# Kernel tuning notes

Measured on AMD Instinct MI355X. Metric: run time of the kernel, lower is better.

## Reference

```python
import jax, jax.numpy as jnp
import numpy as np

B, N, F_IN, F_OUT = 1024, 16, 1024, 4096  # n_nodes=16 and n_heads=1 are structurally fixed by the module


def setup_inputs() -> dict:
    key = jax.random.key(0)
    ks = jax.random.split(key, 7)
    s1 = 1.0 / np.sqrt(F_IN)
    s2 = 1.0 / np.sqrt(F_IN * 16)
    return {
        "x": jax.random.normal(ks[0], (B, N, F_IN), jnp.float32),
        "matrix": jax.random.uniform(ks[1], (B, N, N), jnp.float32),
        "W1": jax.random.uniform(ks[2], (F_IN, F_IN), jnp.float32, -s1, s1),
        "b1": jax.random.uniform(ks[3], (F_IN,), jnp.float32, -s1, s1),
        "W_mlp": jax.random.uniform(ks[4], (F_OUT, F_IN * 16), jnp.float32, -s2, s2),
        "b_mlp": jax.random.uniform(ks[5], (F_OUT,), jnp.float32, -s2, s2),
        "a_param": jnp.float32(5.0),
    }


def _l2norm(v):
    # matches F.normalize(p=2, dim=-1, eps=1e-12)
    n = jnp.maximum(jnp.linalg.norm(v, axis=-1, keepdims=True), 1e-12)
    return v / n


def _forward(x, matrix, W1, b1, W_mlp, b_mlp, a_param):
    Bc, n, f = x.shape  # n_heads = 1, n_hidden = f
    wg = x @ W1.T + b1                                    # [B,n,f]
    gs = _l2norm(x)                                       # g_reshaped (H=1)
    gt = _l2norm(wg)                                      # g_transposed
    e = jnp.einsum('bik,bjk->bij', gs, gt)[..., None]     # [B,n,n,1] cosine scores
    eye = jnp.eye(n, dtype=x.dtype)[None, :, :, None]
    e = e * (1.0 + eye * a_param)                         # boost diagonal
    a_scores = e                                          # pre-softmax scores (used below)
    esm = jax.nn.softmax(e, axis=1)                       # softmax over dim=1
    m = matrix[..., None]                                 # [B,n,n,1]
    # MPUGAT message passing
    from_i = jnp.einsum('bitp,btkp->bikp', esm, m)        # [B,n,n,1]
    diag = jnp.einsum('bkkp->bkp', m)                     # diagonal of matrix
    from_j = esm * diag[:, None, :, :]                    # '...jkp,...kkp->...jkp'
    e2 = jnp.einsum('bikp,bjkp->bijp', from_i, from_j)    # [B,n,n,1]
    e2 = 0.5 * (e2 + jnp.transpose(e2, (0, 2, 1, 3)))
    # attention readout with PRE-softmax scores a_scores
    g = x.reshape(Bc, n, 1, f)                            # [B,n,H=1,f]
    attn = jnp.tanh(jnp.einsum('bjhf,bjih->bihf', g, a_scores))  # [B,n,1,f]
    out = attn.reshape(Bc, -1) @ W_mlp.T + b_mlp          # [B,F_OUT]
    out = jnp.broadcast_to(out[:, None, :], (Bc, 16, out.shape[-1]))  # repeat(1,16,1)
    return out, e2, m


def reference(x, matrix, W1, b1, W_mlp, b_mlp, a_param):
    return _forward(x, matrix, W1, b1, W_mlp, b_mlp, a_param)
```

## Files before the change

### kernel.cpp

```cpp
#include <hip/hip_runtime.h>
#include <math.h>

typedef short short8 __attribute__((ext_vector_type(8)));
typedef float f32x4 __attribute__((ext_vector_type(4)));
typedef unsigned short us4 __attribute__((ext_vector_type(4)));
typedef unsigned int u32x4 __attribute__((ext_vector_type(4)));
typedef unsigned short u16;
typedef unsigned int u32;

#define GAS __attribute__((address_space(1)))
#define LAS __attribute__((address_space(3)))

static __device__ __forceinline__ u16 f2bf(float f) {
    union { float f; u32 u; } v; v.f = f;
    u32 r = v.u + 0x7FFFu + ((v.u >> 16) & 1u);
    return (u16)(r >> 16);
}

static __device__ __forceinline__ u32 pk2(float a, float b) {
    return (u32)f2bf(a) | ((u32)f2bf(b) << 16);
}

static __device__ __forceinline__ u32 cvtpk(float lo, float hi) {
    u32 r;
    asm("v_cvt_pk_bf16_f32 %0, %1, %2" : "=v"(r) : "v"(lo), "v"(hi));
    return r;
}

static __device__ __forceinline__ float bf2f(u16 h) {
    union { u32 u; float f; } v; v.u = ((u32)h) << 16;
    return v.f;
}

static __device__ __forceinline__ void gll16(const void* g, void* l) {
    __builtin_amdgcn_global_load_lds((const GAS void*)g, (LAS void*)l, 16, 0, 0);
}

__global__ __launch_bounds__(256) void k_cvt_x(const float* __restrict__ x,
                                               u16* __restrict__ xb,
                                               float* __restrict__ xinv) {
    const int row = blockIdx.x, t = threadIdx.x;
    const f32x4 v = *(const f32x4*)(x + (size_t)row * 1024 + 4 * t);
    u32* dst = (u32*)(xb + (size_t)row * 1024 + 4 * t);
    dst[0] = pk2(v.x, v.y); dst[1] = pk2(v.z, v.w);
    float s = v.x * v.x + v.y * v.y + v.z * v.z + v.w * v.w;
#pragma unroll
    for (int off = 1; off < 64; off <<= 1) s += __shfl_xor(s, off, 64);
    __shared__ float red[4];
    if ((t & 63) == 0) red[t >> 6] = s;
    __syncthreads();
    if (t == 0)
        xinv[row] = 1.0f / fmaxf(sqrtf(red[0] + red[1] + red[2] + red[3]), 1e-12f);
}

__global__ __launch_bounds__(256) void k_cvt(const float* __restrict__ in,
                                             u16* __restrict__ out) {
    const size_t i = (size_t)blockIdx.x * 256 + threadIdx.x;
    const f32x4 v = *(const f32x4*)(in + 4 * i);
    u32* dst = (u32*)(out + 4 * i);
    dst[0] = pk2(v.x, v.y); dst[1] = pk2(v.z, v.w);
}

#define MFMA16(a, b, c) __builtin_amdgcn_mfma_f32_16x16x32_bf16(a, b, c, 0, 0, 0)
#define SBAR() __builtin_amdgcn_s_barrier()
#define LGKM0() do { asm volatile("s_waitcnt lgkmcnt(0)" ::: "memory"); __builtin_amdgcn_sched_barrier(0); } while (0)
#define SCHED0() __builtin_amdgcn_sched_barrier(0)
#define VMW4 asm volatile("s_waitcnt vmcnt(4)" ::: "memory")
#define VMW2 asm volatile("s_waitcnt vmcnt(2)" ::: "memory")
#define VMW0 asm volatile("s_waitcnt vmcnt(0)" ::: "memory")
#define VMW8L asm volatile("s_waitcnt vmcnt(8) lgkmcnt(0)" ::: "memory")
#define LGKML asm volatile("s_waitcnt lgkmcnt(0)" ::: "memory")
#define VMNOP do {} while (0)

#define DO_TILE(ISS, VMA, VMB, VMD)                                           \
  do {                                                                        \
    short8 Af[4][2], Bf0[2][2], Bf1[2][2];                                    \
    _Pragma("unroll") for (int m = 0; m < 4; ++m) {                           \
      Af[m][0] = *(const short8*)(la + rpA[m] + sw0);                         \
      Af[m][1] = *(const short8*)(la + rpA[m] + sw1);                         \
    }                                                                         \
    _Pragma("unroll") for (int n = 0; n < 2; ++n) {                           \
      Bf0[n][0] = *(const short8*)(lb + rpB[n] + sw0);                        \
      Bf0[n][1] = *(const short8*)(lb + rpB[n] + sw1);                        \
    }                                                                         \
    if (ISS) { gll16(AG + (saO00 + knx), danext + ldst);                      \
               gll16(AG + (saO01 + knx), danext + 4096 + ldst); }             \
    SBAR(); LGKM0();                                                          \
    __builtin_amdgcn_s_setprio(1);                                            \
    _Pragma("unroll") for (int m = 0; m < 4; ++m)                             \
      _Pragma("unroll") for (int n = 0; n < 2; ++n) {                         \
        acc[m][n] = MFMA16(Af[m][0], Bf0[n][0], acc[m][n]);                   \
        acc[m][n] = MFMA16(Af[m][1], Bf0[n][1], acc[m][n]);                   \
      }                                                                       \
    __builtin_amdgcn_s_setprio(0); SCHED0(); VMA; SBAR();                     \
    _Pragma("unroll") for (int n = 0; n < 2; ++n) {                           \
      Bf1[n][0] = *(const short8*)(lb + rpB[n + 2] + sw0);                    \
      Bf1[n][1] = *(const short8*)(lb + rpB[n + 2] + sw1);                    \
    }                                                                         \
    if (ISS) { gll16(BG + (sbO00 + knx), dbnext + ldst);                      \
               gll16(BG + (sbO01 + knx), dbnext + 4096 + ldst); }             \
    SBAR(); LGKM0();                                                          \
    __builtin_amdgcn_s_setprio(1);                                            \
    _Pragma("unroll") for (int m = 0; m < 4; ++m)                             \
      _Pragma("unroll") for (int n = 0; n < 2; ++n) {                         \
        acc[m][n + 2] = MFMA16(Af[m][0], Bf1[n][0], acc[m][n + 2]);           \
        acc[m][n + 2] = MFMA16(Af[m][1], Bf1[n][1], acc[m][n + 2]);           \
      }                                                                       \
    __builtin_amdgcn_s_setprio(0); SCHED0(); VMB; SBAR();                     \
    _Pragma("unroll") for (int m = 0; m < 4; ++m) {                           \
      Af[m][0] = *(const short8*)(la + rpA[m + 4] + sw0);                     \
      Af[m][1] = *(const short8*)(la + rpA[m + 4] + sw1);                     \
    }                                                                         \
    if (ISS) { gll16(BG + (sbO10 + knx), dbnext + 8192 + ldst);               \
               gll16(BG + (sbO11 + knx), dbnext + 8192 + 4096 + ldst); }      \
    SBAR(); LGKM0();                                                          \
    __builtin_amdgcn_s_setprio(1);                                            \
    _Pragma("unroll") for (int m = 0; m < 4; ++m)                             \
      _Pragma("unroll") for (int n = 0; n < 2; ++n) {                         \
        acc[m + 4][n] = MFMA16(Af[m][0], Bf0[n][0], acc[m + 4][n]);           \
        acc[m + 4][n] = MFMA16(Af[m][1], Bf0[n][1], acc[m + 4][n]);           \
      }                                                                       \
    __builtin_amdgcn_s_setprio(0); SCHED0(); SBAR();                          \
    if (ISS) { gll16(AG + (saO10 + knx), danext + 8192 + ldst);               \
               gll16(AG + (saO11 + knx), danext + 8192 + 4096 + ldst); }      \
    __builtin_amdgcn_s_setprio(1);                                            \
    _Pragma("unroll") for (int m = 0; m < 4; ++m)                             \
      _Pragma("unroll") for (int n = 0; n < 2; ++n) {                         \
        acc[m + 4][n + 2] = MFMA16(Af[m][1], Bf1[n][1], acc[m + 4][n + 2]);   \
        acc[m + 4][n + 2] = MFMA16(Af[m][0], Bf1[n][0], acc[m + 4][n + 2]);   \
      }                                                                       \
    __builtin_amdgcn_s_setprio(0); SCHED0(); VMD; SBAR();                     \
  } while (0)

#define DO_TILE2(ISS, KNXA, KNX2, WEND)                                       \
  do {                                                                        \
    short8 Af[4][2], Bf0[2][2], Bf1[2][2];                                    \
    _Pragma("unroll") for (int m = 0; m < 4; ++m) {                           \
      Af[m][0] = *(const short8*)(la + rpA[m] + sw0);                         \
      Af[m][1] = *(const short8*)(la + rpA[m] + sw1);                         \
    }                                                                         \
    _Pragma("unroll") for (int n = 0; n < 2; ++n) {                           \
      Bf0[n][0] = *(const short8*)(lb + rpB[n] + sw0);                        \
      Bf0[n][1] = *(const short8*)(lb + rpB[n] + sw1);                        \
    }                                                                         \
    if (ISS) {                                                                \
      gll16(AG + (saO00 + (KNXA)), danext + ldst);                            \
      gll16(AG + (saO01 + (KNXA)), danext + 4096 + ldst);                     \
      gll16(AG + (saO10 + (KNXA)), danext + 8192 + ldst);                     \
      gll16(AG + (saO11 + (KNXA)), danext + 8192 + 4096 + ldst);              \
    }                                                                         \
    SBAR(); LGKM0();                                                          \
    __builtin_amdgcn_s_setprio(1);                                            \
    _Pragma("unroll") for (int m = 0; m < 4; ++m)                             \
      _Pragma("unroll") for (int n = 0; n < 2; ++n) {                         \
        acc[m][n] = MFMA16(Af[m][0], Bf0[n][0], acc[m][n]);                   \
        acc[m][n] = MFMA16(Af[m][1], Bf0[n][1], acc[m][n]);                   \
      }                                                                       \
    __builtin_amdgcn_s_setprio(0); SCHED0(); SBAR();                          \
    _Pragma("unroll") for (int n = 0; n < 2; ++n) {                           \
      Bf1[n][0] = *(const short8*)(lb + rpB[n + 2] + sw0);                    \
      Bf1[n][1] = *(const short8*)(lb + rpB[n + 2] + sw1);                    \
    }                                                                         \
    SBAR(); LGKM0();                                                          \
    __builtin_amdgcn_s_setprio(1);                                            \
    _Pragma("unroll") for (int m = 0; m < 4; ++m)                             \
      _Pragma("unroll") for (int n = 0; n < 2; ++n) {                         \
        acc[m][n + 2] = MFMA16(Af[m][0], Bf1[n][0], acc[m][n + 2]);           \
        acc[m][n + 2] = MFMA16(Af[m][1], Bf1[n][1], acc[m][n + 2]);           \
      }                                                                       \
    __builtin_amdgcn_s_setprio(0); SCHED0(); SBAR();                          \
    _Pragma("unroll") for (int m = 0; m < 4; ++m) {                           \
      Af[m][0] = *(const short8*)(la + rpA[m + 4] + sw0);                     \
      Af[m][1] = *(const short8*)(la + rpA[m + 4] + sw1);                     \
    }                                                                         \
    SBAR(); LGKM0();                                                          \
    __builtin_amdgcn_s_setprio(1);                                            \
    _Pragma("unroll") for (int m = 0; m < 4; ++m)                             \
      _Pragma("unroll") for (int n = 0; n < 2; ++n) {                         \
        acc[m + 4][n] = MFMA16(Af[m][0], Bf0[n][0], acc[m + 4][n]);           \
        acc[m + 4][n] = MFMA16(Af[m][1], Bf0[n][1], acc[m + 4][n]);           \
      }                                                                       \
    __builtin_amdgcn_s_setprio(0);                                            \
    if (ISS) {                                                                \
      _Pragma("unroll") for (int c = 0; c < 2; ++c) {                         \
        u32x4 wv;                                                             \
        wv.x = cvtpk(bn[2 * c].x, bn[2 * c].y);                               \
        wv.y = cvtpk(bn[2 * c].z, bn[2 * c].w);                               \
        wv.z = cvtpk(bn[2 * c + 1].x, bn[2 * c + 1].y);                       \
        wv.w = cvtpk(bn[2 * c + 1].z, bn[2 * c + 1].w);                       \
        *(u32x4*)(dbnext + c * 4096 + (tid << 3)) = wv;                       \
        bn[2 * c]     = *(const f32x4*)(BGf + bro[c] + (KNX2) + swsrc);       \
        bn[2 * c + 1] = *(const f32x4*)(BGf + bro[c] + (KNX2) + swsrc + 4);   \
      }                                                                       \
    }                                                                         \
    SBAR();                                                                   \
    __builtin_amdgcn_s_setprio(1);                                            \
    _Pragma("unroll") for (int m = 0; m < 4; ++m)                             \
      _Pragma("unroll") for (int n = 0; n < 2; ++n) {                         \
        acc[m + 4][n + 2] = MFMA16(Af[m][0], Bf1[n][0], acc[m + 4][n + 2]);   \
        acc[m + 4][n + 2] = MFMA16(Af[m][1], Bf1[n][1], acc[m + 4][n + 2]);   \
      }                                                                       \
    __builtin_amdgcn_s_setprio(0);                                            \
    if (ISS) {                                                                \
      _Pragma("unroll") for (int c = 2; c < 4; ++c) {                         \
        u32x4 wv;                                                             \
        wv.x = cvtpk(bn[2 * c].x, bn[2 * c].y);                               \
        wv.y = cvtpk(bn[2 * c].z, bn[2 * c].w);                               \
        wv.z = cvtpk(bn[2 * c + 1].x, bn[2 * c + 1].y);                       \
        wv.w = cvtpk(bn[2 * c + 1].z, bn[2 * c + 1].w);                       \
        *(u32x4*)(dbnext + c * 4096 + (tid << 3)) = wv;                       \
        bn[2 * c]     = *(const f32x4*)(BGf + bro[c] + (KNX2) + swsrc);       \
        bn[2 * c + 1] = *(const f32x4*)(BGf + bro[c] + (KNX2) + swsrc + 4);   \
      }                                                                       \
    }                                                                         \
    WEND; SBAR();                                                             \
  } while (0)

__global__ __launch_bounds__(512, 2) void k_gemm1_8ph(const u16* __restrict__ AG,
                                                      const u16* __restrict__ BG,
                                                      const float* __restrict__ bias,
                                                      u16* __restrict__ C,
                                                      float* __restrict__ wgn2) {
    __shared__ __align__(16) u16 LsA[2][16384];
    __shared__ __align__(16) u16 LsB[2][16384];
    const int K = 1024, NT = 16;
    const int lin = blockIdx.x;
    const int w = (lin & 7) * 32 + (lin >> 3);
    const int n0 = (w & 3) * 256;
    const int m0 = (w >> 2) * 256;

    const int tid = threadIdx.x, wave = tid >> 6, lane = tid & 63;
    const int lr = lane & 15, kq = lane >> 4;
    const int wr = wave >> 2, wc = wave & 3;

    const int trow = tid >> 3;
    const u32 swsrc = (u32)(((tid & 7) ^ (trow & 7)) * 8);
    const u32 saO00 = (u32)(m0 + 0 + trow) * (u32)K + swsrc;
    const u32 saO01 = (u32)(m0 + 128 + trow) * (u32)K + swsrc;
    const u32 saO10 = (u32)(m0 + 64 + trow) * (u32)K + swsrc;
    const u32 saO11 = (u32)(m0 + 192 + trow) * (u32)K + swsrc;
    const int q0 = trow, q1 = 64 + trow;
    const u32 sbO00 = (u32)(n0 + (q0 >> 5) * 64 + (q0 & 31)) * (u32)K + swsrc;
    const u32 sbO01 = (u32)(n0 + (q1 >> 5) * 64 + (q1 & 31)) * (u32)K + swsrc;
    const u32 sbO10 = (u32)(n0 + (q0 >> 5) * 64 + 32 + (q0 & 31)) * (u32)K + swsrc;
    const u32 sbO11 = (u32)(n0 + (q1 >> 5) * 64 + 32 + (q1 & 31)) * (u32)K + swsrc;
    const u32 ldst = (u32)wave * 512;

    int rpA[8], rpB[4];
#pragma unroll
    for (int mf = 0; mf < 8; ++mf)
        rpA[mf] = ((mf >> 2) * 128 + wr * 64 + (mf & 3) * 16 + lr) << 6;
#pragma unroll
    for (int nf = 0; nf < 4; ++nf)
        rpB[nf] = ((nf >> 1) * 128 + wc * 32 + (nf & 1) * 16 + lr) << 6;
    const int sw0 = ((0 + kq) ^ (lr & 7)) * 8;
    const int sw1 = ((4 + kq) ^ (lr & 7)) * 8;

    f32x4 acc[8][4] = {};

    gll16(AG + saO00, &LsA[0][0] + ldst);
    gll16(AG + saO01, &LsA[0][0] + 4096 + ldst);
    gll16(BG + sbO00, &LsB[0][0] + ldst);
    gll16(BG + sbO01, &LsB[0][0] + 4096 + ldst);
    gll16(BG + sbO10, &LsB[0][0] + 8192 + ldst);
    gll16(BG + sbO11, &LsB[0][0] + 8192 + 4096 + ldst);
    gll16(AG + saO10, &LsA[0][0] + 8192 + ldst);
    gll16(AG + saO11, &LsA[0][0] + 8192 + 4096 + ldst);
    VMW4;
    SBAR();

    int cur = 0;
    u32 ko = 64;
    for (int T = 0; T < NT - 1; ++T) {
        const u16* la = &LsA[cur][0];
        const u16* lb = &LsB[cur][0];
        u16* danext = &LsA[cur ^ 1][0];
        u16* dbnext = &LsB[cur ^ 1][0];
        const u32 knx = ko;
        DO_TILE(1, VMW4, VMW4, VMW4);
        cur ^= 1;
        ko += 64;
    }
    {
        const u16* la = &LsA[cur][0];
        const u16* lb = &LsB[cur][0];
        u16* danext = &LsA[cur ^ 1][0];
        u16* dbnext = &LsB[cur ^ 1][0];
        const u32 knx = 0;
        (void)danext; (void)dbnext;
        DO_TILE(0, VMW2, VMW0, VMNOP);
    }

    const int col0 = n0 + wc * 64;
    const int row0 = m0 + wr * 128;
    float bcol[4];
#pragma unroll
    for (int nf = 0; nf < 4; ++nf) bcol[nf] = bias[col0 + nf * 16 + lr];
#pragma unroll
    for (int mf = 0; mf < 8; ++mf) {
#pragma unroll
        for (int r = 0; r < 4; ++r) {
            const int row = row0 + mf * 16 + kq * 4 + r;
            float nrm = 0.f;
#pragma unroll
            for (int nf = 0; nf < 4; ++nf) {
                float v = acc[mf][nf][r] + bcol[nf];
                C[(size_t)row * 1024 + col0 + nf * 16 + lr] = f2bf(v);
                nrm += v * v;
            }
#pragma unroll
            for (int off = 1; off < 16; off <<= 1) nrm += __shfl_xor(nrm, off, 64);
            if (lr == 0) atomicAdd(&wgn2[row], nrm);
        }
    }
}

__global__ __launch_bounds__(512, 2) void k_gemm2_8ph(const u16* __restrict__ AG,
                                                      const float* __restrict__ BGf,
                                                      u16* __restrict__ part) {
    __shared__ __align__(16) u16 LsA[2][16384];
    __shared__ __align__(16) u16 LsB[2][16384];
    const int K = 16384, NT = 64;
    const int lin = blockIdx.x;
    const int w = (lin & 7) * 32 + (lin >> 3);
    const int m0 = (w & 3) * 256;
    const int z = (w >> 2) & 3;
    const int n0 = (w >> 4) * 256;
    const int kbeg = z * 4096;

    const int tid = threadIdx.x, wave = tid >> 6, lane = tid & 63;
    const int lr = lane & 15, kq = lane >> 4;
    const int wr = wave >> 2, wc = wave & 3;

    const int trow = tid >> 3;
    const u32 swsrc = (u32)(((tid & 7) ^ (trow & 7)) * 8);
    const u32 saO00 = (u32)(m0 + 0 + trow) * (u32)K + (u32)kbeg + swsrc;
    const u32 saO01 = (u32)(m0 + 128 + trow) * (u32)K + (u32)kbeg + swsrc;
    const u32 saO10 = (u32)(m0 + 64 + trow) * (u32)K + (u32)kbeg + swsrc;
    const u32 saO11 = (u32)(m0 + 192 + trow) * (u32)K + (u32)kbeg + swsrc;
    const int q0 = trow, q1 = 64 + trow;
    size_t bro[4];
    bro[0] = (size_t)(n0 + (q0 >> 5) * 64 + (q0 & 31)) * 16384 + kbeg;
    bro[1] = (size_t)(n0 + (q1 >> 5) * 64 + (q1 & 31)) * 16384 + kbeg;
    bro[2] = bro[0] + 32ull * 16384;
    bro[3] = bro[1] + 32ull * 16384;
    const u32 ldst = (u32)wave * 512;

    int rpA[8], rpB[4];
#pragma unroll
    for (int mf = 0; mf < 8; ++mf)
        rpA[mf] = ((mf >> 2) * 128 + wr * 64 + (mf & 3) * 16 + lr) << 6;
#pragma unroll
    for (int nf = 0; nf < 4; ++nf)
        rpB[nf] = ((nf >> 1) * 128 + wc * 32 + (nf & 1) * 16 + lr) << 6;
    const int sw0 = ((0 + kq) ^ (lr & 7)) * 8;
    const int sw1 = ((4 + kq) ^ (lr & 7)) * 8;

    f32x4 acc[8][4] = {};
    f32x4 bn[8];

    {
#pragma unroll
        for (int c = 0; c < 4; ++c) {
            bn[2 * c]     = *(const f32x4*)(BGf + bro[c] + swsrc);
            bn[2 * c + 1] = *(const f32x4*)(BGf + bro[c] + swsrc + 4);
        }
        gll16(AG + saO00, &LsA[0][0] + ldst);
        gll16(AG + saO01, &LsA[0][0] + 4096 + ldst);
        gll16(AG + saO10, &LsA[0][0] + 8192 + ldst);
        gll16(AG + saO11, &LsA[0][0] + 8192 + 4096 + ldst);
#pragma unroll
        for (int c = 0; c < 4; ++c) {
            u32x4 wv;
            wv.x = cvtpk(bn[2 * c].x, bn[2 * c].y);
            wv.y = cvtpk(bn[2 * c].z, bn[2 * c].w);
            wv.z = cvtpk(bn[2 * c + 1].x, bn[2 * c + 1].y);
            wv.w = cvtpk(bn[2 * c + 1].z, bn[2 * c + 1].w);
            *(u32x4*)(&LsB[0][0] + c * 4096 + (tid << 3)) = wv;
        }
        asm volatile("s_waitcnt vmcnt(0) lgkmcnt(0)" ::: "memory");
#pragma unroll
        for (int c = 0; c < 4; ++c) {
            bn[2 * c]     = *(const f32x4*)(BGf + bro[c] + 64 + swsrc);
            bn[2 * c + 1] = *(const f32x4*)(BGf + bro[c] + 64 + swsrc + 4);
        }
        SBAR();
    }

    int cur = 0;
    for (int T = 0; T < NT - 1; ++T) {
        const u16* la = &LsA[cur][0];
        const u16* lb = &LsB[cur][0];
        u16* danext = &LsA[cur ^ 1][0];
        u16* dbnext = &LsB[cur ^ 1][0];
        const u32 knxa = (u32)(T + 1) * 64;
        const u32 knx2 = (T + 2 < NT) ? (u32)(T + 2) * 64 : 0u;
        DO_TILE2(1, knxa, knx2, VMW8L);
        cur ^= 1;
    }
    {
        const u16* la = &LsA[cur][0];
        const u16* lb = &LsB[cur][0];
        u16* danext = &LsA[cur ^ 1][0];
        u16* dbnext = &LsB[cur ^ 1][0];
        (void)danext; (void)dbnext;
        DO_TILE2(0, 0u, 0u, VMNOP);
    }

    u16* po = part + (size_t)z * 4194304ull;
    const int col0 = n0 + wc * 64;
    const int row0 = m0 + wr * 128;
#pragma unroll
    for (int mf = 0; mf < 8; ++mf)
#pragma unroll
        for (int r = 0; r < 4; ++r) {
            const int row = row0 + mf * 16 + kq * 4 + r;
#pragma unroll
            for (int nf = 0; nf < 4; ++nf)
                po[(size_t)row * 4096 + col0 + nf * 16 + lr] = f2bf(acc[mf][nf][r]);
        }
}

__global__ __launch_bounds__(64) void k_batch(const u16* __restrict__ xb,
                                              const u16* __restrict__ wgb,
                                              const float* __restrict__ xinv,
                                              const float* __restrict__ wgn2,
                                              const float* __restrict__ matrix,
                                              const float* __restrict__ a_param,
                                              float* __restrict__ ascores,
                                              float* __restrict__ e2_out,
                                              float* __restrict__ m_out) {
    const int b = blockIdx.x, l = threadIdx.x;
    const int j = l & 15, ig = (l >> 4) * 4;
    const size_t roff = (size_t)(b * 16 + j) * 1024 + (l >> 4) * 8;
    f32x4 acc0 = {}, acc1 = {};
#pragma unroll
    for (int kt = 0; kt < 1024; kt += 64) {
        short8 xa0 = *(const short8*)(xb + roff + kt);
        short8 wa0 = *(const short8*)(wgb + roff + kt);
        short8 xa1 = *(const short8*)(xb + roff + kt + 32);
        short8 wa1 = *(const short8*)(wgb + roff + kt + 32);
        acc0 = __builtin_amdgcn_mfma_f32_16x16x32_bf16(xa0, wa0, acc0, 0, 0, 0);
        acc1 = __builtin_amdgcn_mfma_f32_16x16x32_bf16(xa1, wa1, acc1, 0, 0, 0);
    }
    const float inw = 1.0f / fmaxf(sqrtf(wgn2[b * 16 + j]), 1e-12f);
    const float boost = 1.0f + a_param[0];
    float e[4];
#pragma unroll
    for (int r = 0; r < 4; ++r) {
        const int i = ig + r;
        float v = (acc0[r] + acc1[r]) * xinv[b * 16 + i] * inw;
        if (i == j) v *= boost;
        e[r] = v;
        ascores[(size_t)b * 256 + i * 16 + j] = v;
    }
    float mx = fmaxf(fmaxf(e[0], e[1]), fmaxf(e[2], e[3]));
    mx = fmaxf(mx, __shfl_xor(mx, 16, 64));
    mx = fmaxf(mx, __shfl_xor(mx, 32, 64));
    float p[4], s = 0.f;
#pragma unroll
    for (int r = 0; r < 4; ++r) { p[r] = __expf(e[r] - mx); s += p[r]; }
    s += __shfl_xor(s, 16, 64);
    s += __shfl_xor(s, 32, 64);
    const float invs = 1.0f / s;

    __shared__ float esm_l[16 * 17];
    __shared__ float fi_l[16 * 17];
    __shared__ float e2_l[16 * 17];
    __shared__ float m_l[256];
#pragma unroll
    for (int r = 0; r < 4; ++r) esm_l[(ig + r) * 17 + j] = p[r] * invs;
    const f32x4 mv = *(const f32x4*)(matrix + (size_t)b * 256 + 4 * l);
    *(f32x4*)(m_l + 4 * l) = mv;
    *(f32x4*)(m_out + (size_t)b * 256 + 4 * l) = mv;
    __syncthreads();
    float fi[4] = {0, 0, 0, 0};
#pragma unroll
    for (int t = 0; t < 16; ++t) {
        const float mk = m_l[t * 16 + j];
#pragma unroll
        for (int r = 0; r < 4; ++r) fi[r] += esm_l[(ig + r) * 17 + t] * mk;
    }
#pragma unroll
    for (int r = 0; r < 4; ++r) fi_l[(ig + r) * 17 + j] = fi[r];
    __syncthreads();
    float e2v[4] = {0, 0, 0, 0};
#pragma unroll
    for (int kk = 0; kk < 16; ++kk) {
        const float wgt = esm_l[j * 17 + kk] * m_l[kk * 16 + kk];
#pragma unroll
        for (int r = 0; r < 4; ++r) e2v[r] += fi_l[(ig + r) * 17 + kk] * wgt;
    }
#pragma unroll
    for (int r = 0; r < 4; ++r) e2_l[(ig + r) * 17 + j] = e2v[r];
    __syncthreads();
#pragma unroll
    for (int r = 0; r < 4; ++r) {
        const int i = ig + r;
        e2_out[(size_t)b * 256 + i * 16 + j] = 0.5f * (e2_l[i * 17 + j] + e2_l[j * 17 + i]);
    }
}

__global__ __launch_bounds__(256) void k_attn(const float* __restrict__ x,
                                              const float* __restrict__ ascores,
                                              u16* __restrict__ attn_bf) {
    __shared__ float xl[16][256];
    __shared__ float as_l[256];
    const int b = blockIdx.y, f0 = blockIdx.x * 256, t = threadIdx.x;
    as_l[t] = ascores[(size_t)b * 256 + t];
#pragma unroll
    for (int jj = 0; jj < 16; ++jj)
        xl[jj][t] = x[((size_t)b * 16 + jj) * 1024 + f0 + t];
    __syncthreads();
    float accv[16] = {};
#pragma unroll
    for (int jj = 0; jj < 16; ++jj) {
        const float xv = xl[jj][t];
#pragma unroll
        for (int i = 0; i < 16; ++i) accv[i] = fmaf(as_l[jj * 16 + i], xv, accv[i]);
    }
#pragma unroll
    for (int i = 0; i < 16; ++i)
        attn_bf[((size_t)b * 16 + i) * 1024 + f0 + t] = f2bf(tanhf(accv[i]));
}

__global__ __launch_bounds__(256) void k_bcast(const u16* __restrict__ p,
                                               const float* __restrict__ bias,
                                               float* __restrict__ out) {
    const size_t i = (size_t)blockIdx.x * 256 + threadIdx.x;
    const int o4 = (int)(i & 1023);
    const int b = (int)(i >> 14);
    const size_t src = (size_t)b * 4096 + (size_t)o4 * 4;
    f32x4 r = *(const f32x4*)(bias + (size_t)o4 * 4);
#pragma unroll
    for (int z = 0; z < 4; ++z) {
        us4 v = *(const us4*)(p + (size_t)z * 4194304ull + src);
        r.x += bf2f(v.x); r.y += bf2f(v.y); r.z += bf2f(v.z); r.w += bf2f(v.w);
    }
    *(f32x4*)(out + i * 4) = r;
}

extern "C" void kernel_launch(void* const* d_in, const int* in_sizes, int n_in,
                              void* d_out, int out_size, void* d_ws, size_t ws_size,
                              hipStream_t stream) {
    const float* x      = (const float*)d_in[0];
    const float* matrix = (const float*)d_in[1];
    const float* W1     = (const float*)d_in[2];
    const float* b1     = (const float*)d_in[3];
    const float* W_mlp  = (const float*)d_in[4];
    const float* b_mlp  = (const float*)d_in[5];
    const float* a_par  = (const float*)d_in[6];
    float* out = (float*)d_out;

    char* ws = (char*)d_ws;
    size_t off = 0;
    auto alloc = [&](size_t bytes) {
        char* p = ws + off;
        off += (bytes + 255) & ~(size_t)255;
        return p;
    };
    u16*   x_bf  = (u16*)alloc(16384ull * 1024 * 2);
    u16*   wg_bf = (u16*)alloc(16384ull * 1024 * 2);
    u16*   w1_bf = (u16*)alloc(1024ull * 1024 * 2);
    float* xinv  = (float*)alloc(16384ull * 4);
    float* wgn2  = (float*)alloc(16384ull * 4);
    float* ascr  = (float*)alloc(1024ull * 256 * 4);
    u16*   attn_bf = x_bf;
    u16*   part    = wg_bf;
    float* e2_out = out + 67108864ull;
    float* m_out  = out + 67371008ull;

    hipMemsetAsync(wgn2, 0, 16384 * 4, stream);
    k_cvt_x<<<16384, 256, 0, stream>>>(x, x_bf, xinv);
    k_cvt<<<1024, 256, 0, stream>>>(W1, w1_bf);
    k_gemm1_8ph<<<256, 512, 0, stream>>>(x_bf, w1_bf, b1, wg_bf, wgn2);
    k_batch<<<1024, 64, 0, stream>>>(x_bf, wg_bf, xinv, wgn2, matrix, a_par,
                                     ascr, e2_out, m_out);
    k_attn<<<dim3(4, 1024), 256, 0, stream>>>(x, ascr, attn_bf);
    k_gemm2_8ph<<<256, 512, 0, stream>>>(attn_bf, W_mlp, part);
    k_bcast<<<65536, 256, 0, stream>>>(part, b_mlp, out);
}
```

Measured before the change: 393.5 us.

## Deepen gemm2 fp32 B prefetch and fuse batch scoring with attention readout

The second GEMM now double-buffers the fp32 W_mlp register prefetch (bnA/bnB, two tiles ahead), splits the A-tile async loads across phases, reorders the MFMA k-loops, and uses 32-bit row offsets. This is meant to hide global load latency behind the MFMAs. Separately, k_batch and k_attn are merged into one 256-thread kernel. It keeps the scores in shared memory and reads bf16 x instead of fp32 x, which removes a launch, the ascores round trip and the fp32 reread of x. The cost is that the attention readout now uses bf16-rounded x, and most threads sit idle during the 64-thread softmax section.

```diff
diff --git a/kernel.cpp b/kernel.cpp
--- a/kernel.cpp
+++ b/kernel.cpp
@@ -69,6 +69,7 @@
 #define VMW2 asm volatile("s_waitcnt vmcnt(2)" ::: "memory")
 #define VMW0 asm volatile("s_waitcnt vmcnt(0)" ::: "memory")
 #define VMW8L asm volatile("s_waitcnt vmcnt(8) lgkmcnt(0)" ::: "memory")
+#define VMW0L asm volatile("s_waitcnt vmcnt(0) lgkmcnt(0)" ::: "memory")
 #define LGKML asm volatile("s_waitcnt lgkmcnt(0)" ::: "memory")
 #define VMNOP do {} while (0)
 
@@ -132,7 +133,7 @@
     __builtin_amdgcn_s_setprio(0); SCHED0(); VMD; SBAR();                     \
   } while (0)
 
-#define DO_TILE2(ISS, KNXA, KNX2, WEND)                                       \
+#define GT2(ISSA, ISSB, BNO, KNXA, KNXB, WAITX)                               \
   do {                                                                        \
     short8 Af[4][2], Bf0[2][2], Bf1[2][2];                                    \
     _Pragma("unroll") for (int m = 0; m < 4; ++m) {                           \
@@ -143,31 +144,27 @@
       Bf0[n][0] = *(const short8*)(lb + rpB[n] + sw0);                        \
       Bf0[n][1] = *(const short8*)(lb + rpB[n] + sw1);                        \
     }                                                                         \
-    if (ISS) {                                                                \
-      gll16(AG + (saO00 + (KNXA)), danext + ldst);                            \
-      gll16(AG + (saO01 + (KNXA)), danext + 4096 + ldst);                     \
-      gll16(AG + (saO10 + (KNXA)), danext + 8192 + ldst);                     \
-      gll16(AG + (saO11 + (KNXA)), danext + 8192 + 4096 + ldst);              \
-    }                                                                         \
+    if (ISSA) { gll16(AG + (saO00 + (KNXA)), danext + ldst);                  \
+                gll16(AG + (saO01 + (KNXA)), danext + 4096 + ldst); }         \
     SBAR(); LGKM0();                                                          \
     __builtin_amdgcn_s_setprio(1);                                            \
-    _Pragma("unroll") for (int m = 0; m < 4; ++m)                             \
-      _Pragma("unroll") for (int n = 0; n < 2; ++n) {                         \
-        acc[m][n] = MFMA16(Af[m][0], Bf0[n][0], acc[m][n]);                   \
-        acc[m][n] = MFMA16(Af[m][1], Bf0[n][1], acc[m][n]);                   \
-      }                                                                       \
+    _Pragma("unroll") for (int k = 0; k < 2; ++k)                             \
+      _Pragma("unroll") for (int m = 0; m < 4; ++m)                           \
+        _Pragma("unroll") for (int n = 0; n < 2; ++n)                         \
+          acc[m][n] = MFMA16(Af[m][k], Bf0[n][k], acc[m][n]);                 \
     __builtin_amdgcn_s_setprio(0); SCHED0(); SBAR();                          \
     _Pragma("unroll") for (int n = 0; n < 2; ++n) {                           \
       Bf1[n][0] = *(const short8*)(lb + rpB[n + 2] + sw0);                    \
       Bf1[n][1] = *(const short8*)(lb + rpB[n + 2] + sw1);                    \
     }                                                                         \
+    if (ISSA) { gll16(AG + (saO10 + (KNXA)), danext + 8192 + ldst);           \
+                gll16(AG + (saO11 + (KNXA)), danext + 8192 + 4096 + ldst); }  \
     SBAR(); LGKM0();                                                          \
     __builtin_amdgcn_s_setprio(1);                                            \
-    _Pragma("unroll") for (int m = 0; m < 4; ++m)                             \
-      _Pragma("unroll") for (int n = 0; n < 2; ++n) {                         \
-        acc[m][n + 2] = MFMA16(Af[m][0], Bf1[n][0], acc[m][n + 2]);           \
-        acc[m][n + 2] = MFMA16(Af[m][1], Bf1[n][1], acc[m][n + 2]);           \
-      }                                                                       \
+    _Pragma("unroll") for (int k = 0; k < 2; ++k)                             \
+      _Pragma("unroll") for (int m = 0; m < 4; ++m)                           \
+        _Pragma("unroll") for (int n = 0; n < 2; ++n)                         \
+          acc[m][n + 2] = MFMA16(Af[m][k], Bf1[n][k], acc[m][n + 2]);         \
     __builtin_amdgcn_s_setprio(0); SCHED0(); SBAR();                          \
     _Pragma("unroll") for (int m = 0; m < 4; ++m) {                           \
       Af[m][0] = *(const short8*)(la + rpA[m + 4] + sw0);                     \
@@ -175,45 +172,41 @@
     }                                                                         \
     SBAR(); LGKM0();                                                          \
     __builtin_amdgcn_s_setprio(1);                                            \
-    _Pragma("unroll") for (int m = 0; m < 4; ++m)                             \
-      _Pragma("unroll") for (int n = 0; n < 2; ++n) {                         \
-        acc[m + 4][n] = MFMA16(Af[m][0], Bf0[n][0], acc[m + 4][n]);           \
-        acc[m + 4][n] = MFMA16(Af[m][1], Bf0[n][1], acc[m + 4][n]);           \
+    _Pragma("unroll") for (int k = 0; k < 2; ++k)                             \
+      _Pragma("unroll") for (int m = 0; m < 4; ++m)                           \
+        _Pragma("unroll") for (int n = 0; n < 2; ++n)                         \
+          acc[m + 4][n] = MFMA16(Af[m][k], Bf0[n][k], acc[m + 4][n]);         \
+    __builtin_amdgcn_s_setprio(0); SCHED0();                                  \
+    _Pragma("unroll") for (int c = 0; c < 2; ++c) {                           \
+      u32x4 wv;                                                               \
+      wv.x = cvtpk(BNO[2 * c].x, BNO[2 * c].y);                               \
+      wv.y = cvtpk(BNO[2 * c].z, BNO[2 * c].w);                               \
+      wv.z = cvtpk(BNO[2 * c + 1].x, BNO[2 * c + 1].y);                       \
+      wv.w = cvtpk(BNO[2 * c + 1].z, BNO[2 * c + 1].w);                       \
+      *(u32x4*)(dbnext + c * 4096 + (tid << 3)) = wv;                         \
+    }                                                                         \
+    SBAR();                                                                   \
+    __builtin_amdgcn_s_setprio(1);                                            \
+    _Pragma("unroll") for (int k = 0; k < 2; ++k)                             \
+      _Pragma("unroll") for (int m = 0; m < 4; ++m)                           \
+        _Pragma("unroll") for (int n = 0; n < 2; ++n)                         \
+          acc[m + 4][n + 2] = MFMA16(Af[m][k], Bf1[n][k], acc[m + 4][n + 2]); \
+    __builtin_amdgcn_s_setprio(0); SCHED0();                                  \
+    _Pragma("unroll") for (int c = 2; c < 4; ++c) {                           \
+      u32x4 wv;                                                               \
+      wv.x = cvtpk(BNO[2 * c].x, BNO[2 * c].y);                               \
+      wv.y = cvtpk(BNO[2 * c].z, BNO[2 * c].w);                               \
+      wv.z = cvtpk(BNO[2 * c + 1].x, BNO[2 * c + 1].y);                       \
+      wv.w = cvtpk(BNO[2 * c + 1].z, BNO[2 * c + 1].w);                       \
+      *(u32x4*)(dbnext + c * 4096 + (tid << 3)) = wv;                         \
+    }                                                                         \
+    if (ISSB) {                                                               \
+      _Pragma("unroll") for (int c = 0; c < 4; ++c) {                         \
+        BNO[2 * c]     = *(const f32x4*)(BGf + bro[c] + (KNXB) + swsrc);      \
+        BNO[2 * c + 1] = *(const f32x4*)(BGf + bro[c] + (KNXB) + swsrc + 4);  \
       }                                                                       \
-    __builtin_amdgcn_s_setprio(0);                                            \
-    if (ISS) {                                                                \
-      _Pragma("unroll") for (int c = 0; c < 2; ++c) {                         \
-        u32x4 wv;                                                             \
-        wv.x = cvtpk(bn[2 * c].x, bn[2 * c].y);                               \
-        wv.y = cvtpk(bn[2 * c].z, bn[2 * c].w);                               \
-        wv.z = cvtpk(bn[2 * c + 1].x, bn[2 * c + 1].y);                       \
-        wv.w = cvtpk(bn[2 * c + 1].z, bn[2 * c + 1].w);                       \
-        *(u32x4*)(dbnext + c * 4096 + (tid << 3)) = wv;                       \
-        bn[2 * c]     = *(const f32x4*)(BGf + bro[c] + (KNX2) + swsrc);       \
-        bn[2 * c + 1] = *(const f32x4*)(BGf + bro[c] + (KNX2) + swsrc + 4);   \
-      }                                                                       \
-    }                                                                         \
-    SBAR();                                                                   \
-    __builtin_amdgcn_s_setprio(1);                                            \
-    _Pragma("unroll") for (int m = 0; m < 4; ++m)                             \
-      _Pragma("unroll") for (int n = 0; n < 2; ++n) {                         \
-        acc[m + 4][n + 2] = MFMA16(Af[m][0], Bf1[n][0], acc[m + 4][n + 2]);   \
-        acc[m + 4][n + 2] = MFMA16(Af[m][1], Bf1[n][1], acc[m + 4][n + 2]);   \
-      }                                                                       \
-    __builtin_amdgcn_s_setprio(0);                                            \
-    if (ISS) {                                                                \
-      _Pragma("unroll") for (int c = 2; c < 4; ++c) {                         \
-        u32x4 wv;                                                             \
-        wv.x = cvtpk(bn[2 * c].x, bn[2 * c].y);                               \
-        wv.y = cvtpk(bn[2 * c].z, bn[2 * c].w);                               \
-        wv.z = cvtpk(bn[2 * c + 1].x, bn[2 * c + 1].y);                       \
-        wv.w = cvtpk(bn[2 * c + 1].z, bn[2 * c + 1].w);                       \
-        *(u32x4*)(dbnext + c * 4096 + (tid << 3)) = wv;                       \
-        bn[2 * c]     = *(const f32x4*)(BGf + bro[c] + (KNX2) + swsrc);       \
-        bn[2 * c + 1] = *(const f32x4*)(BGf + bro[c] + (KNX2) + swsrc + 4);   \
-      }                                                                       \
-    }                                                                         \
-    WEND; SBAR();                                                             \
+    }                                                                         \
+    WAITX; SBAR();                                                            \
   } while (0)
 
 __global__ __launch_bounds__(512, 2) void k_gemm1_8ph(const u16* __restrict__ AG,
@@ -320,7 +313,7 @@
                                                       u16* __restrict__ part) {
     __shared__ __align__(16) u16 LsA[2][16384];
     __shared__ __align__(16) u16 LsB[2][16384];
-    const int K = 16384, NT = 64;
+    const int K = 16384;
     const int lin = blockIdx.x;
     const int w = (lin & 7) * 32 + (lin >> 3);
     const int m0 = (w & 3) * 256;
@@ -339,11 +332,11 @@
     const u32 saO10 = (u32)(m0 + 64 + trow) * (u32)K + (u32)kbeg + swsrc;
     const u32 saO11 = (u32)(m0 + 192 + trow) * (u32)K + (u32)kbeg + swsrc;
     const int q0 = trow, q1 = 64 + trow;
-    size_t bro[4];
-    bro[0] = (size_t)(n0 + (q0 >> 5) * 64 + (q0 & 31)) * 16384 + kbeg;
-    bro[1] = (size_t)(n0 + (q1 >> 5) * 64 + (q1 & 31)) * 16384 + kbeg;
-    bro[2] = bro[0] + 32ull * 16384;
-    bro[3] = bro[1] + 32ull * 16384;
+    u32 bro[4];
+    bro[0] = (u32)(n0 + (q0 >> 5) * 64 + (q0 & 31)) * 16384u + (u32)kbeg;
+    bro[1] = (u32)(n0 + (q1 >> 5) * 64 + (q1 & 31)) * 16384u + (u32)kbeg;
+    bro[2] = bro[0] + 32u * 16384u;
+    bro[3] = bro[1] + 32u * 16384u;
     const u32 ldst = (u32)wave * 512;
 
     int rpA[8], rpB[4];
@@ -357,13 +350,13 @@
     const int sw1 = ((4 + kq) ^ (lr & 7)) * 8;
 
     f32x4 acc[8][4] = {};
-    f32x4 bn[8];
+    f32x4 bnA[8], bnB[8];
 
     {
 #pragma unroll
         for (int c = 0; c < 4; ++c) {
-            bn[2 * c]     = *(const f32x4*)(BGf + bro[c] + swsrc);
-            bn[2 * c + 1] = *(const f32x4*)(BGf + bro[c] + swsrc + 4);
+            bnA[2 * c]     = *(const f32x4*)(BGf + bro[c] + swsrc);
+            bnA[2 * c + 1] = *(const f32x4*)(BGf + bro[c] + swsrc + 4);
         }
         gll16(AG + saO00, &LsA[0][0] + ldst);
         gll16(AG + saO01, &LsA[0][0] + 4096 + ldst);
@@ -372,39 +365,68 @@
 #pragma unroll
         for (int c = 0; c < 4; ++c) {
             u32x4 wv;
-            wv.x = cvtpk(bn[2 * c].x, bn[2 * c].y);
-            wv.y = cvtpk(bn[2 * c].z, bn[2 * c].w);
-            wv.z = cvtpk(bn[2 * c + 1].x, bn[2 * c + 1].y);
-            wv.w = cvtpk(bn[2 * c + 1].z, bn[2 * c + 1].w);
+            wv.x = cvtpk(bnA[2 * c].x, bnA[2 * c].y);
+            wv.y = cvtpk(bnA[2 * c].z, bnA[2 * c].w);
+            wv.z = cvtpk(bnA[2 * c + 1].x, bnA[2 * c + 1].y);
+            wv.w = cvtpk(bnA[2 * c + 1].z, bnA[2 * c + 1].w);
             *(u32x4*)(&LsB[0][0] + c * 4096 + (tid << 3)) = wv;
         }
-        asm volatile("s_waitcnt vmcnt(0) lgkmcnt(0)" ::: "memory");
 #pragma unroll
         for (int c = 0; c < 4; ++c) {
-            bn[2 * c]     = *(const f32x4*)(BGf + bro[c] + 64 + swsrc);
-            bn[2 * c + 1] = *(const f32x4*)(BGf + bro[c] + 64 + swsrc + 4);
-        }
+            bnA[2 * c]     = *(const f32x4*)(BGf + bro[c] + 64 + swsrc);
+            bnA[2 * c + 1] = *(const f32x4*)(BGf + bro[c] + 64 + swsrc + 4);
+        }
+#pragma unroll
+        for (int c = 0; c < 4; ++c) {
+            bnB[2 * c]     = *(const f32x4*)(BGf + bro[c] + 128 + swsrc);
+            bnB[2 * c + 1] = *(const f32x4*)(BGf + bro[c] + 128 + swsrc + 4);
+        }
+        asm volatile("s_waitcnt vmcnt(16) lgkmcnt(0)" ::: "memory");
         SBAR();
     }
 
     int cur = 0;
-    for (int T = 0; T < NT - 1; ++T) {
-        const u16* la = &LsA[cur][0];
-        const u16* lb = &LsB[cur][0];
-        u16* danext = &LsA[cur ^ 1][0];
-        u16* dbnext = &LsB[cur ^ 1][0];
-        const u32 knxa = (u32)(T + 1) * 64;
-        const u32 knx2 = (T + 2 < NT) ? (u32)(T + 2) * 64 : 0u;
-        DO_TILE2(1, knxa, knx2, VMW8L);
+    for (int T = 0; T < 60; T += 2) {
+        {
+            const u16* la = &LsA[cur][0];
+            const u16* lb = &LsB[cur][0];
+            u16* danext = &LsA[cur ^ 1][0];
+            u16* dbnext = &LsB[cur ^ 1][0];
+            GT2(1, 1, bnA, (u32)(T + 1) * 64, (u32)(T + 3) * 64, VMW8L);
+            cur ^= 1;
+        }
+        {
+            const u16* la = &LsA[cur][0];
+            const u16* lb = &LsB[cur][0];
+            u16* danext = &LsA[cur ^ 1][0];
+            u16* dbnext = &LsB[cur ^ 1][0];
+            GT2(1, 1, bnB, (u32)(T + 2) * 64, (u32)(T + 4) * 64, VMW8L);
+            cur ^= 1;
+        }
+    }
+    {
+        const u16* la = &LsA[cur][0]; const u16* lb = &LsB[cur][0];
+        u16* danext = &LsA[cur ^ 1][0]; u16* dbnext = &LsB[cur ^ 1][0];
+        GT2(1, 1, bnA, 61u * 64, 63u * 64, VMW8L);
         cur ^= 1;
     }
     {
-        const u16* la = &LsA[cur][0];
-        const u16* lb = &LsB[cur][0];
-        u16* danext = &LsA[cur ^ 1][0];
-        u16* dbnext = &LsB[cur ^ 1][0];
-        (void)danext; (void)dbnext;
-        DO_TILE2(0, 0u, 0u, VMNOP);
+        const u16* la = &LsA[cur][0]; const u16* lb = &LsB[cur][0];
+        u16* danext = &LsA[cur ^ 1][0]; u16* dbnext = &LsB[cur ^ 1][0];
+        GT2(1, 0, bnB, 62u * 64, 0u, VMW0L);
+        cur ^= 1;
+    }
+    {
+        const u16* la = &LsA[cur][0]; const u16* lb = &LsB[cur][0];
+        u16* danext = &LsA[cur ^ 1][0]; u16* dbnext = &LsB[cur ^ 1][0];
+        GT2(1, 0, bnA, 63u * 64, 0u, VMW0L);
+        cur ^= 1;
+    }
+    {
+        const u16* la = &LsA[cur][0]; const u16* lb = &LsB[cur][0];
+        u16* danext = &LsA[cur ^ 1][0]; u16* dbnext = &LsB[cur ^ 1][0];
+        (void)danext;
+        GT2(0, 0, bnB, 0u, 0u, LGKML);
     }
 
     u16* po = part + (size_t)z * 4194304ull;
@@ -421,107 +443,126 @@
         }
 }
 
-__global__ __launch_bounds__(64) void k_batch(const u16* __restrict__ xb,
-                                              const u16* __restrict__ wgb,
-                                              const float* __restrict__ xinv,
-                                              const float* __restrict__ wgn2,
-                                              const float* __restrict__ matrix,
-                                              const float* __restrict__ a_param,
-                                              float* __restrict__ ascores,
-                                              float* __restrict__ e2_out,
-                                              float* __restrict__ m_out) {
-    const int b = blockIdx.x, l = threadIdx.x;
-    const int j = l & 15, ig = (l >> 4) * 4;
-    const size_t roff = (size_t)(b * 16 + j) * 1024 + (l >> 4) * 8;
-    f32x4 acc0 = {}, acc1 = {};
-#pragma unroll
-    for (int kt = 0; kt < 1024; kt += 64) {
-        short8 xa0 = *(const short8*)(xb + roff + kt);
-        short8 wa0 = *(const short8*)(wgb + roff + kt);
-        short8 xa1 = *(const short8*)(xb + roff + kt + 32);
-        short8 wa1 = *(const short8*)(wgb + roff + kt + 32);
-        acc0 = __builtin_amdgcn_mfma_f32_16x16x32_bf16(xa0, wa0, acc0, 0, 0, 0);
-        acc1 = __builtin_amdgcn_mfma_f32_16x16x32_bf16(xa1, wa1, acc1, 0, 0, 0);
-    }
-    const float inw = 1.0f / fmaxf(sqrtf(wgn2[b * 16 + j]), 1e-12f);
-    const float boost = 1.0f + a_param[0];
-    float e[4];
-#pragma unroll
-    for (int r = 0; r < 4; ++r) {
-        const int i = ig + r;
-        float v = (acc0[r] + acc1[r]) * xinv[b * 16 + i] * inw;
-        if (i == j) v *= boost;
-        e[r] = v;
-        ascores[(size_t)b * 256 + i * 16 + j] = v;
-    }
-    float mx = fmaxf(fmaxf(e[0], e[1]), fmaxf(e[2], e[3]));
-    mx = fmaxf(mx, __shfl_xor(mx, 16, 64));
-    mx = fmaxf(mx, __shfl_xor(mx, 32, 64));
-    float p[4], s = 0.f;
-#pragma unroll
-    for (int r = 0; r < 4; ++r) { p[r] = __expf(e[r] - mx); s += p[r]; }
-    s += __shfl_xor(s, 16, 64);
-    s += __shfl_xor(s, 32, 64);
-    const float invs = 1.0f / s;
-
+__global__ __launch_bounds__(256) void k_batch_attn(const u16* xb,
+                                                    const u16* __restrict__ wgb,
+                                                    const float* __restrict__ xinv,
+                                                    const float* __restrict__ wgn2,
+                                                    const float* __restrict__ matrix,
+                                                    const float* __restrict__ a_param,
+                                                    float* __restrict__ e2_out,
+                                                    float* __restrict__ m_out,
+                                                    u16* attn_bf) {
+    const int b = blockIdx.x, tid = threadIdx.x;
+    const int wave = tid >> 6, lane = tid & 63;
+    const int j = lane & 15, ig = (lane >> 4) * 4;
+
+    __shared__ float qred[4][64][4];
     __shared__ float esm_l[16 * 17];
     __shared__ float fi_l[16 * 17];
     __shared__ float e2_l[16 * 17];
     __shared__ float m_l[256];
-#pragma unroll
-    for (int r = 0; r < 4; ++r) esm_l[(ig + r) * 17 + j] = p[r] * invs;
-    const f32x4 mv = *(const f32x4*)(matrix + (size_t)b * 256 + 4 * l);
-    *(f32x4*)(m_l + 4 * l) = mv;
-    *(f32x4*)(m_out + (size_t)b * 256 + 4 * l) = mv;
+    __shared__ float as_l[256];
+    __shared__ float xsh[16][256];
+
+    {
+        const size_t roff = (size_t)(b * 16 + j) * 1024 + (lane >> 4) * 8 + wave * 256;
+        f32x4 acc0 = {}, acc1 = {};
+#pragma unroll
+        for (int kt = 0; kt < 256; kt += 64) {
+            short8 xa0 = *(const short8*)(xb + roff + kt);
+            short8 wa0 = *(const short8*)(wgb + roff + kt);
+            short8 xa1 = *(const short8*)(xb + roff + kt + 32);
+            short8 wa1 = *(const short8*)(wgb + roff + kt + 32);
+            acc0 = __builtin_amdgcn_mfma_f32_16x16x32_bf16(xa0, wa0, acc0, 0, 0, 0);
+            acc1 = __builtin_amdgcn_mfma_f32_16x16x32_bf16(xa1, wa1, acc1, 0, 0, 0);
+        }
+#pragma unroll
+        for (int r = 0; r < 4; ++r) qred[wave][lane][r] = acc0[r] + acc1[r];
+    }
     __syncthreads();
-    float fi[4] = {0, 0, 0, 0};
-#pragma unroll
-    for (int t = 0; t < 16; ++t) {
-        const float mk = m_l[t * 16 + j];
-#pragma unroll
-        for (int r = 0; r < 4; ++r) fi[r] += esm_l[(ig + r) * 17 + t] * mk;
-    }
-#pragma unroll
-    for (int r = 0; r < 4; ++r) fi_l[(ig + r) * 17 + j] = fi[r];
+
+    if (tid < 64) {
+        const int l = tid;
+        const float inw = 1.0f / fmaxf(sqrtf(wgn2[b * 16 + j]), 1e-12f);
+        const float boost = 1.0f + a_param[0];
+        float e[4];
+#pragma unroll
+        for (int r = 0; r < 4; ++r) {
+            const int i = ig + r;
+            float v = (qred[0][l][r] + qred[1][l][r] + qred[2][l][r] + qred[3][l][r]) *
+                      xinv[b * 16 + i] * inw;
+            if (i == j) v *= boost;
+            e[r] = v;
+            as_l[i * 16 + j] = v;
+        }
+        float mx = fmaxf(fmaxf(e[0], e[1]), fmaxf(e[2], e[3]));
+        mx = fmaxf(mx, __shfl_xor(mx, 16, 64));
+        mx = fmaxf(mx, __shfl_xor(mx, 32, 64));
+        float p[4], s = 0.f;
+#pragma unroll
+        for (int r = 0; r < 4; ++r) { p[r] = __expf(e[r] - mx); s += p[r]; }
+        s += __shfl_xor(s, 16, 64);
+        s += __shfl_xor(s, 32, 64);
+        const float invs = 1.0f / s;
+#pragma unroll
+        for (int r = 0; r < 4; ++r) esm_l[(ig + r) * 17 + j] = p[r] * invs;
+        const f32x4 mv = *(const f32x4*)(matrix + (size_t)b * 256 + 4 * l);
+        *(f32x4*)(m_l + 4 * l) = mv;
+        *(f32x4*)(m_out + (size_t)b * 256 + 4 * l) = mv;
+    }
     __syncthreads();
-    float e2v[4] = {0, 0, 0, 0};
-#pragma unroll
-    for (int kk = 0; kk < 16; ++kk) {
-        const float wgt = esm_l[j * 17 + kk] * m_l[kk * 16 + kk];
-#pragma unroll
-        for (int r = 0; r < 4; ++r) e2v[r] += fi_l[(ig + r) * 17 + kk] * wgt;
-    }
-#pragma unroll
-    for (int r = 0; r < 4; ++r) e2_l[(ig + r) * 17 + j] = e2v[r];
+    if (tid < 64) {
+        const int l = tid;
+        float fi[4] = {0, 0, 0, 0};
+#pragma unroll
+        for (int t = 0; t < 16; ++t) {
+            const float mk = m_l[t * 16 + j];
+#pragma unroll
+            for (int r = 0; r < 4; ++r) fi[r] += esm_l[(ig + r) * 17 + t] * mk;
+        }
+#pragma unroll
+        for (int r = 0; r < 4; ++r) fi_l[(ig + r) * 17 + j] = fi[r];
+        (void)l;
+    }
     __syncthreads();
-#pragma unroll
-    for (int r = 0; r < 4; ++r) {
-        const int i = ig + r;
-        e2_out[(size_t)b * 256 + i * 16 + j] = 0.5f * (e2_l[i * 17 + j] + e2_l[j * 17 + i]);
-    }
-}
-
-__global__ __launch_bounds__(256) void k_attn(const float* __restrict__ x,
-                                              const float* __restrict__ ascores,
-                                              u16* __restrict__ attn_bf) {
-    __shared__ float xl[16][256];
-    __shared__ float as_l[256];
-    const int b = blockIdx.y, f0 = blockIdx.x * 256, t = threadIdx.x;
-    as_l[t] = ascores[(size_t)b * 256 + t];
-#pragma unroll
-    for (int jj = 0; jj < 16; ++jj)
-        xl[jj][t] = x[((size_t)b * 16 + jj) * 1024 + f0 + t];
+    if (tid < 64) {
+        float e2v[4] = {0, 0, 0, 0};
+#pragma unroll
+        for (int kk = 0; kk < 16; ++kk) {
+            const float wgt = esm_l[j * 17 + kk] * m_l[kk * 16 + kk];
+#pragma unroll
+            for (int r = 0; r < 4; ++r) e2v[r] += fi_l[(ig + r) * 17 + kk] * wgt;
+        }
+#pragma unroll
+        for (int r = 0; r < 4; ++r) e2_l[(ig + r) * 17 + j] = e2v[r];
+    }
     __syncthreads();
-    float accv[16] = {};
-#pragma unroll
-    for (int jj = 0; jj < 16; ++jj) {
-        const float xv = xl[jj][t];
-#pragma unroll
-        for (int i = 0; i < 16; ++i) accv[i] = fmaf(as_l[jj * 16 + i], xv, accv[i]);
-    }
-#pragma unroll
-    for (int i = 0; i < 16; ++i)
-        attn_bf[((size_t)b * 16 + i) * 1024 + f0 + t] = f2bf(tanhf(accv[i]));
+    if (tid < 64) {
+#pragma unroll
+        for (int r = 0; r < 4; ++r) {
+            const int i = ig + r;
+            e2_out[(size_t)b * 256 + i * 16 + j] =
+                0.5f * (e2_l[i * 17 + j] + e2_l[j * 17 + i]);
+        }
+    }
+
+    for (int ch = 0; ch < 4; ++ch) {
+        __syncthreads();
+#pragma unroll
+        for (int jj = 0; jj < 16; ++jj)
+            xsh[jj][tid] = bf2f(xb[((size_t)b * 16 + jj) * 1024 + ch * 256 + tid]);
+        __syncthreads();
+        float accv[16] = {};
+#pragma unroll
+        for (int jj = 0; jj < 16; ++jj) {
+            const float xv = xsh[jj][tid];
+#pragma unroll
+            for (int i = 0; i < 16; ++i) accv[i] = fmaf(as_l[jj * 16 + i], xv, accv[i]);
+        }
+#pragma unroll
+        for (int i = 0; i < 16; ++i)
+            attn_bf[((size_t)b * 16 + i) * 1024 + ch * 256 + tid] = f2bf(tanhf(accv[i]));
+    }
 }
 
 __global__ __launch_bounds__(256) void k_bcast(const u16* __restrict__ p,
@@ -564,7 +605,6 @@
     u16*   w1_bf = (u16*)alloc(1024ull * 1024 * 2);
     float* xinv  = (float*)alloc(16384ull * 4);
     float* wgn2  = (float*)alloc(16384ull * 4);
-    float* ascr  = (float*)alloc(1024ull * 256 * 4);
     u16*   attn_bf = x_bf;
     u16*   part    = wg_bf;
     float* e2_out = out + 67108864ull;
@@ -574,9 +614,8 @@
     k_cvt_x<<<16384, 256, 0, stream>>>(x, x_bf, xinv);
     k_cvt<<<1024, 256, 0, stream>>>(W1, w1_bf);
     k_gemm1_8ph<<<256, 512, 0, stream>>>(x_bf, w1_bf, b1, wg_bf, wgn2);
-    k_batch<<<1024, 64, 0, stream>>>(x_bf, wg_bf, xinv, wgn2, matrix, a_par,
-                                     ascr, e2_out, m_out);
-    k_attn<<<dim3(4, 1024), 256, 0, stream>>>(x, ascr, attn_bf);
+    k_batch_attn<<<1024, 256, 0, stream>>>(x_bf, wg_bf, xinv, wgn2, matrix, a_par,
+                                           e2_out, m_out, attn_bf);
     k_gemm2_8ph<<<256, 512, 0, stream>>>(attn_bf, W_mlp, part);
     k_bcast<<<65536, 256, 0, stream>>>(part, b_mlp, out);
 }
```

Measured after the change: 638.5 us. 1.62x slower.
